# Optimization experiments

Measured on AMD Instinct MI355X. Metric: run time of the kernel, lower is better.

Reference implementation:

```python
import jax, jax.numpy as jnp
import numpy as np
import math

N_EMBD = 1024
N_HEAD = 16
HEAD_DIM = N_EMBD // N_HEAD

def setup_inputs() -> dict:
    key = jax.random.key(0)
    ks = jax.random.split(key, 9)
    B, T, C = 2, 2048, N_EMBD
    s = 1.0 / math.sqrt(C)
    return {
        "x": jax.random.normal(ks[0], (B, T, C), dtype=jnp.float32),
        "Wq": jax.random.normal(ks[1], (C, C), dtype=jnp.float32) * s,
        "bq": jnp.zeros((C,), dtype=jnp.float32),
        "Wk": jax.random.normal(ks[2], (C, C), dtype=jnp.float32) * s,
        "bk": jnp.zeros((C,), dtype=jnp.float32),
        "Wv": jax.random.normal(ks[3], (C, C), dtype=jnp.float32) * s,
        "bv": jnp.zeros((C,), dtype=jnp.float32),
        "Wp": jax.random.normal(ks[4], (C, C), dtype=jnp.float32) * s,
        "bp": jnp.zeros((C,), dtype=jnp.float32),
    }

def reference(x, Wq, bq, Wk, bk, Wv, bv, Wp, bp):
    B, T, C = x.shape
    H, D = N_HEAD, HEAD_DIM
    q = (x @ Wq + bq).reshape(B, T, H, D).transpose(0, 2, 1, 3)  # [B,H,T,D]
    k = (x @ Wk + bk).reshape(B, T, H, D).transpose(0, 2, 1, 3)
    v = (x @ Wv + bv).reshape(B, T, H, D).transpose(0, 2, 1, 3)
    att = jnp.einsum('bhqd,bhkd->bhqk', q, k) / math.sqrt(D)
    causal = jnp.tril(jnp.ones((T, T), dtype=bool))
    att = jnp.where(causal, att, -jnp.inf)
    att = jax.nn.softmax(att, axis=-1)
    att = jnp.nan_to_num(att)
    y = jnp.einsum('bhqk,bhkd->bhqd', att, v)
    y = y.transpose(0, 2, 1, 3).reshape(B, T, C)
    return y @ Wp + bp
```

## Files before the change

kernel.cpp:

```cpp
#include <hip/hip_runtime.h>
#include <hip/hip_bf16.h>
#include <stdint.h>

typedef unsigned short u16;
typedef __attribute__((ext_vector_type(8))) short short8;
typedef __attribute__((ext_vector_type(4))) float f32x4;

static __device__ __forceinline__ u16 f2bf(float f) {
  unsigned u = __builtin_bit_cast(unsigned, f);
  u += 0x7fffu + ((u >> 16) & 1u);
  return (u16)(u >> 16);
}

static __device__ __forceinline__ unsigned cvtpk(float lo, float hi) {
  unsigned r;
  asm("v_cvt_pk_bf16_f32 %0, %1, %2" : "=v"(r) : "v"(lo), "v"(hi));
  return r;
}

static __device__ __forceinline__ void gload16(const u16* g, u16* l) {
  __builtin_amdgcn_global_load_lds(
      (__attribute__((address_space(1))) void*)const_cast<u16*>(g),
      (__attribute__((address_space(3))) void*)l, 16, 0, 0);
}

__global__ __launch_bounds__(256) void prep_kernel(
    const float* __restrict__ x, const float* __restrict__ Wq,
    const float* __restrict__ Wk, const float* __restrict__ Wv,
    const float* __restrict__ Wp, u16* __restrict__ xb, u16* __restrict__ wt) {
  __shared__ float tile[64][65];
  int b = blockIdx.x;
  if (b < 2048) {
    size_t i = (size_t)b * 256 + threadIdx.x;
    const float4* xp = (const float4*)x + i * 2;
    float4 a = xp[0], v = xp[1];
    union { u16 u[8]; int4 q; } r;
    r.u[0] = f2bf(a.x); r.u[1] = f2bf(a.y); r.u[2] = f2bf(a.z); r.u[3] = f2bf(a.w);
    r.u[4] = f2bf(v.x); r.u[5] = f2bf(v.y); r.u[6] = f2bf(v.z); r.u[7] = f2bf(v.w);
    *(int4*)(xb + i * 8) = r.q;
  } else {
    int wb = b - 2048;
    int wz = wb >> 8, r8 = wb & 255;
    const float* W = (wz == 0) ? Wq : (wz == 1) ? Wk : (wz == 2) ? Wv : Wp;
    int n0 = (r8 & 15) * 64, k0 = (r8 >> 4) * 64;
    int tx = threadIdx.x & 63, ty = threadIdx.x >> 6;
#pragma unroll
    for (int r = 0; r < 16; ++r)
      tile[ty + 4 * r][tx] = W[(size_t)(k0 + ty + 4 * r) * 1024 + n0 + tx];
    __syncthreads();
    u16* dst = wt + (size_t)wz * 1024 * 1024;
#pragma unroll
    for (int r = 0; r < 16; ++r) {
      int n = ty + 4 * r;
      dst[(size_t)(n0 + n) * 1024 + k0 + tx] = f2bf(tile[tx][n]);
    }
  }
}

template <int EPI>
__global__ __launch_bounds__(256, 2) void gemm128_kernel(
    const u16* __restrict__ A, const u16* __restrict__ Bt, int Kdim,
    int GM, int GN, int RM, int RN,
    u16* __restrict__ qd, u16* __restrict__ kd, u16* __restrict__ vd,
    const float* __restrict__ bq, const float* __restrict__ bk,
    const float* __restrict__ bv, float* __restrict__ outf,
    const float* __restrict__ bias1) {
  __shared__ u16 Alds[2 * 8192];
  __shared__ u16 Blds[2 * 8192];
  int tid = threadIdx.x;
  int lane = tid & 63, w = tid >> 6;
  int l15 = lane & 15, lg = lane >> 4;
  int flat = blockIdx.x;
  int xcd = flat & 7, idx = flat >> 3;
  int rnc = GN / RN;
  int rm = (xcd / rnc) * RM, rn = (xcd % rnc) * RN;
  int im = idx % RM, in_ = idx / RM;
  int m0 = (rm + im) * 128, n0 = (rn + in_) * 128;
  int wm = (w >> 1) * 64, wn = (w & 1) * 64;
  int srow = lane >> 3;
  int colsw = ((lane & 7) * 8) ^ ((srow & 7) * 8);

  const u16* pA[4];
  const u16* pB[4];
  int dls[4];
#pragma unroll
  for (int j = 0; j < 4; ++j) {
    int issue = w * 4 + j;
    int row = issue * 8 + srow;
    pA[j] = A + (size_t)(m0 + row) * Kdim + colsw;
    pB[j] = Bt + (size_t)(n0 + row) * Kdim + colsw;
    dls[j] = issue * 512;
  }
  int kx = (l15 & 7) << 4;
  int ofs0 = (lg * 16) ^ kx, ofs1 = (64 + lg * 16) ^ kx;
  int rbA = (wm + l15) * 128, rbB = (wn + l15) * 128;

  f32x4 acc[4][4] = {};
  {
#pragma unroll
    for (int j = 0; j < 4; ++j) {
      gload16(pA[j], Alds + dls[j]);
      gload16(pB[j], Blds + dls[j]);
      pA[j] += 64; pB[j] += 64;
    }
  }
  int cur = 0;
  for (int kt = 0; kt < Kdim; kt += 64) {
    __syncthreads();
    if (kt + 64 < Kdim) {
      u16* Ad = Alds + (cur ^ 1) * 8192;
      u16* Bd = Blds + (cur ^ 1) * 8192;
#pragma unroll
      for (int j = 0; j < 4; ++j) {
        gload16(pA[j], Ad + dls[j]);
        gload16(pB[j], Bd + dls[j]);
        pA[j] += 64; pB[j] += 64;
      }
    }
    const char* Al = (const char*)Alds + cur * 16384;
    const char* Bl = (const char*)Blds + cur * 16384;
    __builtin_amdgcn_s_setprio(1);
#pragma unroll
    for (int kk = 0; kk < 2; ++kk) {
      int o_ = kk ? ofs1 : ofs0;
      short8 a[4], b[4];
#pragma unroll
      for (int mt = 0; mt < 4; ++mt)
        a[mt] = *(const short8*)(Al + (rbA + o_) + mt * 2048);
#pragma unroll
      for (int nt = 0; nt < 4; ++nt)
        b[nt] = *(const short8*)(Bl + (rbB + o_) + nt * 2048);
#pragma unroll
      for (int mt = 0; mt < 4; ++mt)
#pragma unroll
        for (int nt = 0; nt < 4; ++nt)
          acc[mt][nt] = __builtin_amdgcn_mfma_f32_16x16x32_bf16(a[mt], b[nt],
                                                                acc[mt][nt], 0, 0, 0);
    }
    __builtin_amdgcn_s_setprio(0);
    cur ^= 1;
  }
  if (EPI == 0) {
#pragma unroll
    for (int nt = 0; nt < 4; ++nt) {
      int n = n0 + wn + nt * 16 + l15;
      int wi = n >> 10, nn = n & 1023, h = nn >> 6, d = nn & 63;
      const float* bb = (wi == 0) ? bq : (wi == 1) ? bk : bv;
      float bval = bb[nn];
      if (wi == 2) {
#pragma unroll
        for (int mt = 0; mt < 4; ++mt) {
          int m = m0 + wm + mt * 16 + lg * 4;
          int mb = m >> 11, t = m & 2047;
          unsigned lo = cvtpk(acc[mt][nt][0] + bval, acc[mt][nt][1] + bval);
          unsigned hi = cvtpk(acc[mt][nt][2] + bval, acc[mt][nt][3] + bval);
          *(uint2*)&vd[((size_t)(mb * 16 + h) * 64 + d) * 2048 + t] =
              make_uint2(lo, hi);
        }
      } else {
        u16* dst = (wi == 0) ? qd : kd;
#pragma unroll
        for (int mt = 0; mt < 4; ++mt) {
#pragma unroll
          for (int i = 0; i < 4; ++i) {
            int m = m0 + wm + mt * 16 + lg * 4 + i;
            int mb = m >> 11, t = m & 2047;
            dst[((size_t)(mb * 16 + h) * 2048 + t) * 64 + d] =
                f2bf(acc[mt][nt][i] + bval);
          }
        }
      }
    }
  } else {
#pragma unroll
    for (int nt = 0; nt < 4; ++nt) {
      int n = n0 + wn + nt * 16 + l15;
      float bval = bias1[n];
#pragma unroll
      for (int mt = 0; mt < 4; ++mt) {
#pragma unroll
        for (int i = 0; i < 4; ++i) {
          int m = m0 + wm + mt * 16 + lg * 4 + i;
          outf[(size_t)m * 1024 + n] = acc[mt][nt][i] + bval;
        }
      }
    }
  }
}

__global__ __launch_bounds__(256, 4) void fattn_kernel(const u16* __restrict__ qb,
                                                       const u16* __restrict__ kb,
                                                       const u16* __restrict__ vt,
                                                       u16* __restrict__ y) {
  __shared__ u16 Klds[2 * 4096];
  __shared__ u16 Vlds[2 * 4096];
  __shared__ u16 Plds[4 * 1024];
  int tid = threadIdx.x, lane = tid & 63, w = tid >> 6;
  int l15 = lane & 15, lg = lane >> 4;
  int flat = blockIdx.x;
  int bh = flat & 31;
  int qt = 31 - (flat >> 5);
  size_t base = (size_t)bh * 2048 * 64;
  int mb = bh >> 4, h = bh & 15;
  const float SC = 0.125f * 1.44269504088896340736f;
  const float NINF = -__builtin_inff();

  int r0 = tid >> 3, c0 = ((tid & 7) * 8) ^ ((r0 & 7) << 3);
  int r1 = (256 + tid) >> 3, c1 = ((tid & 7) * 8) ^ ((r1 & 7) << 3);
  const u16* pK0 = kb + base + (size_t)r0 * 64 + c0;
  const u16* pK1 = kb + base + (size_t)r1 * 64 + c1;
  const u16* pV0 = vt + base + (size_t)r0 * 2048 + c0;
  const u16* pV1 = vt + base + (size_t)r1 * 2048 + c1;
  int dk0 = w * 512, dk1 = (256 + w * 64) * 8;
  int kx = (l15 & 7) << 4;
  int rb0 = l15 * 128 + ((lg * 16) ^ kx);
  int rb1 = l15 * 128 + ((64 + lg * 16) ^ kx);
  char* pbase = (char*)Plds + w * 2048;
  int pw0 = l15 * 128 + ((lg * 8) ^ kx);
  int pw1 = l15 * 128 + ((32 + lg * 8) ^ kx);
  int pw2 = l15 * 128 + ((64 + lg * 8) ^ kx);
  int pw3 = l15 * 128 + ((96 + lg * 8) ^ kx);

  int qw = qt * 64 + w * 16;
  int qr = qw + l15;
  short8 qf[2];
#pragma unroll
  for (int kk = 0; kk < 2; ++kk)
    qf[kk] = *(const short8*)&qb[base + (size_t)qr * 64 + kk * 32 + lg * 8];
  f32x4 o[4] = {};
  float mrow = NINF, lrow = 0.f;
  {
    gload16(pK0, Klds + dk0); gload16(pK1, Klds + dk1);
    gload16(pV0, Vlds + dk0); gload16(pV1, Vlds + dk1);
    pK0 += 4096; pK1 += 4096; pV0 += 64; pV1 += 64;
  }
  int cb = 0;
  int ntiles = qt + 1;
  for (int j = 0; j < ntiles; ++j) {
    __syncthreads();
    if (j + 1 < ntiles) {
      u16* kd_ = Klds + (cb ^ 1) * 4096;
      u16* vd_ = Vlds + (cb ^ 1) * 4096;
      gload16(pK0, kd_ + dk0); gload16(pK1, kd_ + dk1);
      gload16(pV0, vd_ + dk0); gload16(pV1, vd_ + dk1);
      pK0 += 4096; pK1 += 4096; pV0 += 64; pV1 += 64;
    }
    const char* kl = (const char*)Klds + cb * 8192;
    const char* vl = (const char*)Vlds + cb * 8192;
    f32x4 s[4] = {};
    __builtin_amdgcn_s_setprio(1);
#pragma unroll
    for (int kk = 0; kk < 2; ++kk) {
      int o_ = kk ? rb1 : rb0;
      short8 ka[4];
#pragma unroll
      for (int nt = 0; nt < 4; ++nt)
        ka[nt] = *(const short8*)(kl + o_ + nt * 2048);
#pragma unroll
      for (int nt = 0; nt < 4; ++nt)
        s[nt] = __builtin_amdgcn_mfma_f32_16x16x32_bf16(ka[nt], qf[kk], s[nt], 0, 0, 0);
    }
    __builtin_amdgcn_s_setprio(0);
    float rs[16];
    if (j == qt) {
      int k0 = j * 64;
#pragma unroll
      for (int nt = 0; nt < 4; ++nt)
#pragma unroll
        for (int i = 0; i < 4; ++i) {
          int ka_ = k0 + nt * 16 + lg * 4 + i;
          rs[nt * 4 + i] = (ka_ > qr) ? NINF : s[nt][i];
        }
    } else {
#pragma unroll
      for (int nt = 0; nt < 4; ++nt)
#pragma unroll
        for (int i = 0; i < 4; ++i) rs[nt * 4 + i] = s[nt][i];
    }
    float rmax = fmaxf(
        fmaxf(fmaxf(fmaxf(rs[0], rs[1]), fmaxf(rs[2], rs[3])),
              fmaxf(fmaxf(rs[4], rs[5]), fmaxf(rs[6], rs[7]))),
        fmaxf(fmaxf(fmaxf(rs[8], rs[9]), fmaxf(rs[10], rs[11])),
              fmaxf(fmaxf(rs[12], rs[13]), fmaxf(rs[14], rs[15]))));
    float tmax = rmax * SC;
    if (!__all(tmax <= mrow + 8.f)) {
      float t2 = fmaxf(tmax, __shfl_xor(tmax, 16));
      t2 = fmaxf(t2, __shfl_xor(t2, 32));
      float vmax = fmaxf(t2, mrow);
      float scale = exp2f(mrow - vmax);
      mrow = vmax;
      lrow *= scale;
#pragma unroll
      for (int dn = 0; dn < 4; ++dn) o[dn] *= scale;
    }
    float p[16];
#pragma unroll
    for (int u = 0; u < 16; ++u) p[u] = exp2f(fmaf(rs[u], SC, -mrow));
    float pr0 = ((p[0] + p[1]) + (p[2] + p[3])) + ((p[4] + p[5]) + (p[6] + p[7]));
    float pr1 = ((p[8] + p[9]) + (p[10] + p[11])) + ((p[12] + p[13]) + (p[14] + p[15]));
    lrow += pr0 + pr1;
    *(uint2*)(pbase + pw0) = make_uint2(cvtpk(p[0], p[1]), cvtpk(p[2], p[3]));
    *(uint2*)(pbase + pw1) = make_uint2(cvtpk(p[4], p[5]), cvtpk(p[6], p[7]));
    *(uint2*)(pbase + pw2) = make_uint2(cvtpk(p[8], p[9]), cvtpk(p[10], p[11]));
    *(uint2*)(pbase + pw3) = make_uint2(cvtpk(p[12], p[13]), cvtpk(p[14], p[15]));
    __builtin_amdgcn_s_setprio(1);
#pragma unroll
    for (int kk = 0; kk < 2; ++kk) {
      int o_ = kk ? rb1 : rb0;
      short8 ap = *(const short8*)(pbase + o_);
#pragma unroll
      for (int dn = 0; dn < 4; ++dn) {
        short8 bv_ = *(const short8*)(vl + o_ + dn * 2048);
        o[dn] = __builtin_amdgcn_mfma_f32_16x16x32_bf16(bv_, ap, o[dn], 0, 0, 0);
      }
    }
    __builtin_amdgcn_s_setprio(0);
    cb ^= 1;
  }
  lrow += __shfl_xor(lrow, 16);
  lrow += __shfl_xor(lrow, 32);
  float inv = 1.f / lrow;
  size_t rb = ((size_t)(mb * 2048 + qr)) * 1024 + (size_t)h * 64;
#pragma unroll
  for (int dn = 0; dn < 4; ++dn) {
    unsigned lo = cvtpk(o[dn][0] * inv, o[dn][1] * inv);
    unsigned hi = cvtpk(o[dn][2] * inv, o[dn][3] * inv);
    *(uint2*)&y[rb + dn * 16 + lg * 4] = make_uint2(lo, hi);
  }
}

extern "C" void kernel_launch(void* const* d_in, const int* in_sizes, int n_in,
                              void* d_out, int out_size, void* d_ws, size_t ws_size,
                              hipStream_t stream) {
  const float* x  = (const float*)d_in[0];
  const float* Wq = (const float*)d_in[1];
  const float* bq = (const float*)d_in[2];
  const float* Wk = (const float*)d_in[3];
  const float* bk = (const float*)d_in[4];
  const float* Wv = (const float*)d_in[5];
  const float* bv = (const float*)d_in[6];
  const float* Wp = (const float*)d_in[7];
  const float* bp = (const float*)d_in[8];
  float* out = (float*)d_out;
  char* ws = (char*)d_ws;
  u16* xb   = (u16*)(ws);
  u16* wt   = (u16*)(ws + ((size_t)8 << 20));
  u16* qbuf = (u16*)(ws + ((size_t)16 << 20));
  u16* kbuf = (u16*)(ws + ((size_t)24 << 20));
  u16* vtb  = (u16*)(ws + ((size_t)32 << 20));
  u16* ybuf = (u16*)(ws + ((size_t)40 << 20));

  prep_kernel<<<dim3(3072), dim3(256), 0, stream>>>(x, Wq, Wk, Wv, Wp, xb, wt);
  gemm128_kernel<0><<<dim3(768), dim3(256), 0, stream>>>(
      xb, wt, 1024, 32, 24, 8, 12,
      qbuf, kbuf, vtb, bq, bk, bv, (float*)nullptr, (const float*)nullptr);
  fattn_kernel<<<dim3(1024), dim3(256), 0, stream>>>(qbuf, kbuf, vtb, ybuf);
  gemm128_kernel<1><<<dim3(256), dim3(256), 0, stream>>>(
      ybuf, wt + (size_t)3 * 1024 * 1024, 1024, 32, 8, 8, 4,
      (u16*)nullptr, (u16*)nullptr, (u16*)nullptr,
      (const float*)nullptr, (const float*)nullptr, (const float*)nullptr, out, bp);
  (void)in_sizes; (void)n_in; (void)out_size; (void)ws_size;
}
```

Measured before the change: 113.7 us.

## Split GEMM into single-buffered QKV kernel and narrower-tile projection kernel

The templated GEMM is split into two kernels. The QKV GEMM drops double buffering and uses single-buffered LDS with two barriers per k-step, which halves LDS use so more blocks can be resident per CU. The output projection switches to 128x64 tiles with 512 blocks instead of 256, giving more parallelism across CUs for the smaller GEMM. The trade-off is that the QKV kernel loses overlap between global loads and MFMA work, and the narrower projection tiles get less data reuse per block.

```diff
diff --git a/kernel.cpp b/kernel.cpp
--- a/kernel.cpp
+++ b/kernel.cpp
@@ -57,16 +57,14 @@
   }
 }
 
-template <int EPI>
-__global__ __launch_bounds__(256, 2) void gemm128_kernel(
+__global__ __launch_bounds__(256, 2) void gemm_qkv_kernel(
     const u16* __restrict__ A, const u16* __restrict__ Bt, int Kdim,
     int GM, int GN, int RM, int RN,
     u16* __restrict__ qd, u16* __restrict__ kd, u16* __restrict__ vd,
     const float* __restrict__ bq, const float* __restrict__ bk,
-    const float* __restrict__ bv, float* __restrict__ outf,
-    const float* __restrict__ bias1) {
-  __shared__ u16 Alds[2 * 8192];
-  __shared__ u16 Blds[2 * 8192];
+    const float* __restrict__ bv) {
+  __shared__ u16 Alds[8192];
+  __shared__ u16 Blds[8192];
   int tid = threadIdx.x;
   int lane = tid & 63, w = tid >> 6;
   int l15 = lane & 15, lg = lane >> 4;
@@ -96,29 +94,14 @@
   int rbA = (wm + l15) * 128, rbB = (wn + l15) * 128;
 
   f32x4 acc[4][4] = {};
-  {
+  for (int kt = 0; kt < Kdim; kt += 64) {
 #pragma unroll
     for (int j = 0; j < 4; ++j) {
       gload16(pA[j], Alds + dls[j]);
       gload16(pB[j], Blds + dls[j]);
       pA[j] += 64; pB[j] += 64;
     }
-  }
-  int cur = 0;
-  for (int kt = 0; kt < Kdim; kt += 64) {
     __syncthreads();
-    if (kt + 64 < Kdim) {
-      u16* Ad = Alds + (cur ^ 1) * 8192;
-      u16* Bd = Blds + (cur ^ 1) * 8192;
-#pragma unroll
-      for (int j = 0; j < 4; ++j) {
-        gload16(pA[j], Ad + dls[j]);
-        gload16(pB[j], Bd + dls[j]);
-        pA[j] += 64; pB[j] += 64;
-      }
-    }
-    const char* Al = (const char*)Alds + cur * 16384;
-    const char* Bl = (const char*)Blds + cur * 16384;
     __builtin_amdgcn_s_setprio(1);
 #pragma unroll
     for (int kk = 0; kk < 2; ++kk) {
@@ -126,10 +109,10 @@
       short8 a[4], b[4];
 #pragma unroll
       for (int mt = 0; mt < 4; ++mt)
-        a[mt] = *(const short8*)(Al + (rbA + o_) + mt * 2048);
+        a[mt] = *(const short8*)((const char*)Alds + (rbA + o_) + mt * 2048);
 #pragma unroll
       for (int nt = 0; nt < 4; ++nt)
-        b[nt] = *(const short8*)(Bl + (rbB + o_) + nt * 2048);
+        b[nt] = *(const short8*)((const char*)Blds + (rbB + o_) + nt * 2048);
 #pragma unroll
       for (int mt = 0; mt < 4; ++mt)
 #pragma unroll
@@ -138,51 +121,127 @@
                                                                 acc[mt][nt], 0, 0, 0);
     }
     __builtin_amdgcn_s_setprio(0);
-    cur ^= 1;
-  }
-  if (EPI == 0) {
-#pragma unroll
-    for (int nt = 0; nt < 4; ++nt) {
-      int n = n0 + wn + nt * 16 + l15;
-      int wi = n >> 10, nn = n & 1023, h = nn >> 6, d = nn & 63;
-      const float* bb = (wi == 0) ? bq : (wi == 1) ? bk : bv;
-      float bval = bb[nn];
-      if (wi == 2) {
-#pragma unroll
-        for (int mt = 0; mt < 4; ++mt) {
-          int m = m0 + wm + mt * 16 + lg * 4;
+    __syncthreads();
+  }
+#pragma unroll
+  for (int nt = 0; nt < 4; ++nt) {
+    int n = n0 + wn + nt * 16 + l15;
+    int wi = n >> 10, nn = n & 1023, h = nn >> 6, d = nn & 63;
+    const float* bb = (wi == 0) ? bq : (wi == 1) ? bk : bv;
+    float bval = bb[nn];
+    if (wi == 2) {
+#pragma unroll
+      for (int mt = 0; mt < 4; ++mt) {
+        int m = m0 + wm + mt * 16 + lg * 4;
+        int mb = m >> 11, t = m & 2047;
+        unsigned lo = cvtpk(acc[mt][nt][0] + bval, acc[mt][nt][1] + bval);
+        unsigned hi = cvtpk(acc[mt][nt][2] + bval, acc[mt][nt][3] + bval);
+        *(uint2*)&vd[((size_t)(mb * 16 + h) * 64 + d) * 2048 + t] =
+            make_uint2(lo, hi);
+      }
+    } else {
+      u16* dst = (wi == 0) ? qd : kd;
+#pragma unroll
+      for (int mt = 0; mt < 4; ++mt) {
+#pragma unroll
+        for (int i = 0; i < 4; ++i) {
+          int m = m0 + wm + mt * 16 + lg * 4 + i;
           int mb = m >> 11, t = m & 2047;
-          unsigned lo = cvtpk(acc[mt][nt][0] + bval, acc[mt][nt][1] + bval);
-          unsigned hi = cvtpk(acc[mt][nt][2] + bval, acc[mt][nt][3] + bval);
-          *(uint2*)&vd[((size_t)(mb * 16 + h) * 64 + d) * 2048 + t] =
-              make_uint2(lo, hi);
-        }
-      } else {
-        u16* dst = (wi == 0) ? qd : kd;
-#pragma unroll
-        for (int mt = 0; mt < 4; ++mt) {
-#pragma unroll
-          for (int i = 0; i < 4; ++i) {
-            int m = m0 + wm + mt * 16 + lg * 4 + i;
-            int mb = m >> 11, t = m & 2047;
-            dst[((size_t)(mb * 16 + h) * 2048 + t) * 64 + d] =
-                f2bf(acc[mt][nt][i] + bval);
-          }
+          dst[((size_t)(mb * 16 + h) * 2048 + t) * 64 + d] =
+              f2bf(acc[mt][nt][i] + bval);
         }
       }
     }
-  } else {
-#pragma unroll
-    for (int nt = 0; nt < 4; ++nt) {
-      int n = n0 + wn + nt * 16 + l15;
-      float bval = bias1[n];
-#pragma unroll
-      for (int mt = 0; mt < 4; ++mt) {
-#pragma unroll
-        for (int i = 0; i < 4; ++i) {
-          int m = m0 + wm + mt * 16 + lg * 4 + i;
-          outf[(size_t)m * 1024 + n] = acc[mt][nt][i] + bval;
-        }
+  }
+}
+
+__global__ __launch_bounds__(256, 2) void gemm_proj_kernel(
+    const u16* __restrict__ A, const u16* __restrict__ Bt,
+    float* __restrict__ outf, const float* __restrict__ bias1) {
+  __shared__ u16 Alds[2 * 8192];
+  __shared__ u16 Blds[2 * 4096];
+  int tid = threadIdx.x;
+  int lane = tid & 63, w = tid >> 6;
+  int l15 = lane & 15, lg = lane >> 4;
+  int flat = blockIdx.x;
+  int xcd = flat & 7, idx = flat >> 3;
+  int rm = (xcd >> 1) * 8, rn = (xcd & 1) * 8;
+  int m0 = (rm + (idx & 7)) * 128, n0 = (rn + (idx >> 3)) * 64;
+  int wm = (w >> 1) * 64, wn = (w & 1) * 32;
+  int srow = lane >> 3;
+  int colsw = ((lane & 7) * 8) ^ ((srow & 7) * 8);
+
+  const u16* pA[4];
+  int dlsA[4];
+#pragma unroll
+  for (int j = 0; j < 4; ++j) {
+    int issue = w * 4 + j;
+    int row = issue * 8 + srow;
+    pA[j] = A + (size_t)(m0 + row) * 1024 + colsw;
+    dlsA[j] = issue * 512;
+  }
+  const u16* pB[2];
+  int dlsB[2];
+#pragma unroll
+  for (int it = 0; it < 2; ++it) {
+    int chunk = it * 256 + tid;
+    int row = chunk >> 3;
+    int col = ((chunk & 7) * 8) ^ ((row & 7) * 8);
+    pB[it] = Bt + (size_t)(n0 + row) * 1024 + col;
+    dlsB[it] = (it * 256 + w * 64) * 8;
+  }
+  int kx = (l15 & 7) << 4;
+  int ofs0 = (lg * 16) ^ kx, ofs1 = (64 + lg * 16) ^ kx;
+  int rbA = (wm + l15) * 128, rbB = (wn + l15) * 128;
+
+  auto stage = [&](int buf) {
+    u16* Ad = Alds + buf * 8192;
+    u16* Bd = Blds + buf * 4096;
+#pragma unroll
+    for (int j = 0; j < 4; ++j) { gload16(pA[j], Ad + dlsA[j]); pA[j] += 64; }
+#pragma unroll
+    for (int it = 0; it < 2; ++it) { gload16(pB[it], Bd + dlsB[it]); pB[it] += 64; }
+  };
+
+  f32x4 acc[4][2] = {};
+  stage(0);
+  int cur = 0;
+  for (int kt = 0; kt < 1024; kt += 64) {
+    __syncthreads();
+    if (kt + 64 < 1024) stage(cur ^ 1);
+    const char* Al = (const char*)Alds + cur * 16384;
+    const char* Bl = (const char*)Blds + cur * 8192;
+    __builtin_amdgcn_s_setprio(1);
+#pragma unroll
+    for (int kk = 0; kk < 2; ++kk) {
+      int o_ = kk ? ofs1 : ofs0;
+      short8 a[4], b[2];
+#pragma unroll
+      for (int mt = 0; mt < 4; ++mt)
+        a[mt] = *(const short8*)(Al + (rbA + o_) + mt * 2048);
+#pragma unroll
+      for (int nt = 0; nt < 2; ++nt)
+        b[nt] = *(const short8*)(Bl + (rbB + o_) + nt * 2048);
+#pragma unroll
+      for (int mt = 0; mt < 4; ++mt)
+#pragma unroll
+        for (int nt = 0; nt < 2; ++nt)
+          acc[mt][nt] = __builtin_amdgcn_mfma_f32_16x16x32_bf16(a[mt], b[nt],
+                                                                acc[mt][nt], 0, 0, 0);
+    }
+    __builtin_amdgcn_s_setprio(0);
+    cur ^= 1;
+  }
+#pragma unroll
+  for (int nt = 0; nt < 2; ++nt) {
+    int n = n0 + wn + nt * 16 + l15;
+    float bval = bias1[n];
+#pragma unroll
+    for (int mt = 0; mt < 4; ++mt) {
+#pragma unroll
+      for (int i = 0; i < 4; ++i) {
+        int m = m0 + wm + mt * 16 + lg * 4 + i;
+        outf[(size_t)m * 1024 + n] = acc[mt][nt][i] + bval;
       }
     }
   }
@@ -351,13 +410,10 @@
   u16* ybuf = (u16*)(ws + ((size_t)40 << 20));
 
   prep_kernel<<<dim3(3072), dim3(256), 0, stream>>>(x, Wq, Wk, Wv, Wp, xb, wt);
-  gemm128_kernel<0><<<dim3(768), dim3(256), 0, stream>>>(
-      xb, wt, 1024, 32, 24, 8, 12,
-      qbuf, kbuf, vtb, bq, bk, bv, (float*)nullptr, (const float*)nullptr);
+  gemm_qkv_kernel<<<dim3(768), dim3(256), 0, stream>>>(
+      xb, wt, 1024, 32, 24, 8, 12, qbuf, kbuf, vtb, bq, bk, bv);
   fattn_kernel<<<dim3(1024), dim3(256), 0, stream>>>(qbuf, kbuf, vtb, ybuf);
-  gemm128_kernel<1><<<dim3(256), dim3(256), 0, stream>>>(
-      ybuf, wt + (size_t)3 * 1024 * 1024, 1024, 32, 8, 8, 4,
-      (u16*)nullptr, (u16*)nullptr, (u16*)nullptr,
-      (const float*)nullptr, (const float*)nullptr, (const float*)nullptr, out, bp);
+  gemm_proj_kernel<<<dim3(512), dim3(256), 0, stream>>>(
+      ybuf, wt + (size_t)3 * 1024 * 1024, out, bp);
   (void)in_sizes; (void)n_in; (void)out_size; (void)ws_size;
 }
```

Result: faster. 102.4 us (-9.9%).
